# Kernel tuning notes

Hardware: AMD Instinct MI355X
Metric: run time of the kernel (lower is better)

Reference implementation:

```python
import jax, jax.numpy as jnp
import numpy as np

B, R, N, F = 8, 8, 1024, 256


def setup_inputs() -> dict:
    key = jax.random.key(0)
    k1, k2 = jax.random.split(key)
    inputs = jax.random.normal(k1, (B, R, N, F), dtype=jnp.float32)
    Bs = jax.random.normal(k2, (R, F, F), dtype=jnp.float32) * 0.05
    return {"inputs": inputs, "Bs": Bs}


def reference(inputs, Bs):
    # E_r @ B_r : [B,R,N,F] x [R,F,F] -> [B,R,N,F]
    e = jnp.einsum("brnf,rfg->brng", inputs, Bs)
    # (E_r B_r) @ E_r^T : [B,R,N,F] x [B,R,M,F] -> [B,R,N,M]
    scores = jnp.einsum("brng,brmg->brnm", e, inputs)
    return jax.nn.sigmoid(scores)
```

## Files before the change

kernel.cpp:

```cpp
#include <hip/hip_runtime.h>


typedef float   f32x4 __attribute__((ext_vector_type(4)));
typedef _Float16 f16x8 __attribute__((ext_vector_type(8)));

#define WS_E_OFF   0
#define WS_BST_OFF 16777216
#define WS_e_OFF   17301504

__global__ __launch_bounds__(256) void bl_convert(
    const float* __restrict__ E, const float* __restrict__ Bs,
    _Float16* __restrict__ wsE, _Float16* __restrict__ wsBsT) {
  int bid = blockIdx.x, tid = threadIdx.x;
  if (bid < 8192) {
    int cid = (bid << 8) + tid;
    int br  = cid >> 15;
    int rem = cid & 32767;
    int fc  = rem >> 10;
    int n   = rem & 1023;
    const float* src = E + ((size_t)br << 18) + n * 256 + (fc << 3);
    f32x4 v0 = *(const f32x4*)src;
    f32x4 v1 = *(const f32x4*)(src + 4);
    f16x8 h;
    h[0] = (_Float16)v0[0]; h[1] = (_Float16)v0[1];
    h[2] = (_Float16)v0[2]; h[3] = (_Float16)v0[3];
    h[4] = (_Float16)v1[0]; h[5] = (_Float16)v1[1];
    h[6] = (_Float16)v1[2]; h[7] = (_Float16)v1[3];
    *(f16x8*)(wsE + ((size_t)br << 18) + (fc << 13) + (n << 3)) = h;
  } else {
    int cid = ((bid - 8192) << 8) + tid;
    int r   = cid >> 13;
    int rem = cid & 8191;
    int fc  = rem >> 8;
    int g   = rem & 255;
    const float* src = Bs + (r << 16) + (fc << 3) * 256 + g;
    f16x8 h;
#pragma unroll
    for (int j = 0; j < 8; ++j) h[j] = (_Float16)src[j * 256];
    *(f16x8*)(wsBsT + (r << 16) + (fc << 11) + (g << 3)) = h;
  }
}

__global__ __launch_bounds__(256) void bl_gemm1(
    const _Float16* __restrict__ wsE, const _Float16* __restrict__ wsBsT,
    _Float16* __restrict__ wse) {
  __shared__ _Float16 sA[8192];
  __shared__ _Float16 sB[8192];
  int bid = blockIdx.x;
  int br = bid >> 4;
  int t  = bid & 15;
  int n0 = (t >> 1) << 7;
  int g0 = (t & 1) << 7;
  int r  = br & 7;
  int tid  = threadIdx.x;
  int lane = tid & 63, wave = tid >> 6;
  int wm = wave >> 1, wn = wave & 1;
  int quad = lane >> 4, l16 = lane & 15;

  const _Float16* aG = wsE   + ((size_t)br << 18) + (n0 << 3);
  const _Float16* bG = wsBsT + (r << 16) + (g0 << 3);

  f32x4 acc[4][4] = {};

  for (int kk = 0; kk < 4; ++kk) {
    __syncthreads();
#pragma unroll
    for (int i = 0; i < 4; ++i) {
      int c = (i << 8) + tid;
      int kcl = c >> 7, nl = c & 127;
      *(f16x8*)&sA[c << 3] = *(const f16x8*)(aG + (((kk << 3) + kcl) << 13) + (nl << 3));
    }
#pragma unroll
    for (int i = 0; i < 4; ++i) {
      int c = (i << 8) + tid;
      int kcl = c >> 7, gl = c & 127;
      *(f16x8*)&sB[c << 3] = *(const f16x8*)(bG + (((kk << 3) + kcl) << 11) + (gl << 3));
    }
    __syncthreads();
#pragma unroll
    for (int ks = 0; ks < 2; ++ks) {
      int kc = (ks << 2) + quad;
      f16x8 af[4], bf[4];
#pragma unroll
      for (int rt = 0; rt < 4; ++rt)
        af[rt] = *(const f16x8*)&sA[((kc << 7) + (wm << 6) + (rt << 4) + l16) << 3];
#pragma unroll
      for (int ct = 0; ct < 4; ++ct)
        bf[ct] = *(const f16x8*)&sB[((kc << 7) + (wn << 6) + (ct << 4) + l16) << 3];
#pragma unroll
      for (int rt = 0; rt < 4; ++rt)
#pragma unroll
        for (int ct = 0; ct < 4; ++ct)
          acc[rt][ct] = __builtin_amdgcn_mfma_f32_16x16x32_f16(af[rt], bf[ct], acc[rt][ct], 0, 0, 0);
    }
  }
  _Float16* eB = wse + ((size_t)br << 18);
#pragma unroll
  for (int rt = 0; rt < 4; ++rt) {
#pragma unroll
    for (int ct = 0; ct < 4; ++ct) {
      int g  = g0 + (wn << 6) + (ct << 4) + l16;
      int gc = g >> 3, gj = g & 7;
#pragma unroll
      for (int i = 0; i < 4; ++i) {
        int n = n0 + (wm << 6) + (rt << 4) + (quad << 2) + i;
        eB[(gc << 13) + (n << 3) + gj] = (_Float16)acc[rt][ct][i];
      }
    }
  }
}

__global__ __launch_bounds__(256) void bl_gemm2(
    const _Float16* __restrict__ wse, const _Float16* __restrict__ wsE,
    float* __restrict__ out) {
  __shared__ _Float16 sA[8192];
  __shared__ _Float16 sB[8192];
  int bid = blockIdx.x;
  int br = bid >> 6;
  int t  = bid & 63;
  int n0 = (t >> 3) << 7;
  int m0 = (t & 7) << 7;
  int tid  = threadIdx.x;
  int lane = tid & 63, wave = tid >> 6;
  int wm = wave >> 1, wn = wave & 1;
  int quad = lane >> 4, l16 = lane & 15;

  const _Float16* aG = wse + ((size_t)br << 18) + (n0 << 3);
  const _Float16* bG = wsE + ((size_t)br << 18) + (m0 << 3);

  f32x4 acc[4][4] = {};

  for (int kk = 0; kk < 4; ++kk) {
    __syncthreads();
#pragma unroll
    for (int i = 0; i < 4; ++i) {
      int c = (i << 8) + tid;
      int kcl = c >> 7, nl = c & 127;
      *(f16x8*)&sA[c << 3] = *(const f16x8*)(aG + (((kk << 3) + kcl) << 13) + (nl << 3));
    }
#pragma unroll
    for (int i = 0; i < 4; ++i) {
      int c = (i << 8) + tid;
      int kcl = c >> 7, ml = c & 127;
      *(f16x8*)&sB[c << 3] = *(const f16x8*)(bG + (((kk << 3) + kcl) << 13) + (ml << 3));
    }
    __syncthreads();
#pragma unroll
    for (int ks = 0; ks < 2; ++ks) {
      int kc = (ks << 2) + quad;
      f16x8 af[4], bf[4];
#pragma unroll
      for (int rt = 0; rt < 4; ++rt)
        af[rt] = *(const f16x8*)&sA[((kc << 7) + (wm << 6) + (rt << 4) + l16) << 3];
#pragma unroll
      for (int ct = 0; ct < 4; ++ct)
        bf[ct] = *(const f16x8*)&sB[((kc << 7) + (wn << 6) + (ct << 4) + l16) << 3];
#pragma unroll
      for (int rt = 0; rt < 4; ++rt)
#pragma unroll
        for (int ct = 0; ct < 4; ++ct)
          acc[rt][ct] = __builtin_amdgcn_mfma_f32_16x16x32_f16(af[rt], bf[ct], acc[rt][ct], 0, 0, 0);
    }
  }
  float* oB = out + ((size_t)br << 20);
#pragma unroll
  for (int rt = 0; rt < 4; ++rt) {
#pragma unroll
    for (int ct = 0; ct < 4; ++ct) {
      int m = m0 + (wn << 6) + (ct << 4) + l16;
#pragma unroll
      for (int i = 0; i < 4; ++i) {
        int n = n0 + (wm << 6) + (rt << 4) + (quad << 2) + i;
        float x = acc[rt][ct][i];
        float s = __builtin_amdgcn_rcpf(1.0f + __expf(-x));
        oB[((size_t)n << 10) + m] = s;
      }
    }
  }
}

extern "C" void kernel_launch(void* const* d_in, const int* in_sizes, int n_in,
                              void* d_out, int out_size, void* d_ws, size_t ws_size,
                              hipStream_t stream) {
  const float* E  = (const float*)d_in[0];
  const float* Bs = (const float*)d_in[1];
  _Float16* wsE   = (_Float16*)d_ws + WS_E_OFF;
  _Float16* wsBsT = (_Float16*)d_ws + WS_BST_OFF;
  _Float16* wse   = (_Float16*)d_ws + WS_e_OFF;
  float* out = (float*)d_out;

  bl_convert<<<8448, 256, 0, stream>>>(E, Bs, wsE, wsBsT);
  bl_gemm1<<<1024, 256, 0, stream>>>(wsE, wsBsT, wse);
  bl_gemm2<<<4096, 256, 0, stream>>>(wse, wsE, out);
}
```

Measured before the change: 388.8 us.

## Swap MFMA operands for vectorized epilogue stores, prefetch tiles, remap block order

```diff
diff --git a/kernel.cpp b/kernel.cpp
--- a/kernel.cpp
+++ b/kernel.cpp
@@ -1,8 +1,9 @@
 #include <hip/hip_runtime.h>
 
 
-typedef float   f32x4 __attribute__((ext_vector_type(4)));
+typedef float    f32x4 __attribute__((ext_vector_type(4)));
 typedef _Float16 f16x8 __attribute__((ext_vector_type(8)));
+typedef _Float16 f16x4 __attribute__((ext_vector_type(4)));
 
 #define WS_E_OFF   0
 #define WS_BST_OFF 16777216
@@ -46,7 +47,8 @@
     _Float16* __restrict__ wse) {
   __shared__ _Float16 sA[8192];
   __shared__ _Float16 sB[8192];
-  int bid = blockIdx.x;
+  int b0  = blockIdx.x;
+  int bid = ((b0 & 7) << 7) + (b0 >> 3);
   int br = bid >> 4;
   int t  = bid & 15;
   int n0 = (t >> 1) << 7;
@@ -63,18 +65,25 @@
   f32x4 acc[4][4] = {};
 
   for (int kk = 0; kk < 4; ++kk) {
-    __syncthreads();
+    f16x8 va[4], vb[4];
 #pragma unroll
     for (int i = 0; i < 4; ++i) {
       int c = (i << 8) + tid;
       int kcl = c >> 7, nl = c & 127;
-      *(f16x8*)&sA[c << 3] = *(const f16x8*)(aG + (((kk << 3) + kcl) << 13) + (nl << 3));
+      va[i] = *(const f16x8*)(aG + (((kk << 3) + kcl) << 13) + (nl << 3));
     }
 #pragma unroll
     for (int i = 0; i < 4; ++i) {
       int c = (i << 8) + tid;
       int kcl = c >> 7, gl = c & 127;
-      *(f16x8*)&sB[c << 3] = *(const f16x8*)(bG + (((kk << 3) + kcl) << 11) + (gl << 3));
+      vb[i] = *(const f16x8*)(bG + (((kk << 3) + kcl) << 11) + (gl << 3));
+    }
+    __syncthreads();
+#pragma unroll
+    for (int i = 0; i < 4; ++i) {
+      int c = (i << 8) + tid;
+      *(f16x8*)&sA[c << 3] = va[i];
+      *(f16x8*)&sB[c << 3] = vb[i];
     }
     __syncthreads();
 #pragma unroll
@@ -91,21 +100,21 @@
       for (int rt = 0; rt < 4; ++rt)
 #pragma unroll
         for (int ct = 0; ct < 4; ++ct)
-          acc[rt][ct] = __builtin_amdgcn_mfma_f32_16x16x32_f16(af[rt], bf[ct], acc[rt][ct], 0, 0, 0);
+          acc[rt][ct] = __builtin_amdgcn_mfma_f32_16x16x32_f16(bf[ct], af[rt], acc[rt][ct], 0, 0, 0);
     }
   }
   _Float16* eB = wse + ((size_t)br << 18);
 #pragma unroll
   for (int rt = 0; rt < 4; ++rt) {
+    int n = n0 + (wm << 6) + (rt << 4) + l16;
 #pragma unroll
     for (int ct = 0; ct < 4; ++ct) {
-      int g  = g0 + (wn << 6) + (ct << 4) + l16;
+      int g  = g0 + (wn << 6) + (ct << 4) + (quad << 2);
       int gc = g >> 3, gj = g & 7;
-#pragma unroll
-      for (int i = 0; i < 4; ++i) {
-        int n = n0 + (wm << 6) + (rt << 4) + (quad << 2) + i;
-        eB[(gc << 13) + (n << 3) + gj] = (_Float16)acc[rt][ct][i];
-      }
+      f16x4 h;
+#pragma unroll
+      for (int i = 0; i < 4; ++i) h[i] = (_Float16)acc[rt][ct][i];
+      *(f16x4*)(eB + (gc << 13) + (n << 3) + gj) = h;
     }
   }
 }
@@ -115,7 +124,8 @@
     float* __restrict__ out) {
   __shared__ _Float16 sA[8192];
   __shared__ _Float16 sB[8192];
-  int bid = blockIdx.x;
+  int b0  = blockIdx.x;
+  int bid = ((b0 & 7) << 9) + (b0 >> 3);
   int br = bid >> 6;
   int t  = bid & 63;
   int n0 = (t >> 3) << 7;
@@ -131,18 +141,25 @@
   f32x4 acc[4][4] = {};
 
   for (int kk = 0; kk < 4; ++kk) {
-    __syncthreads();
+    f16x8 va[4], vb[4];
 #pragma unroll
     for (int i = 0; i < 4; ++i) {
       int c = (i << 8) + tid;
       int kcl = c >> 7, nl = c & 127;
-      *(f16x8*)&sA[c << 3] = *(const f16x8*)(aG + (((kk << 3) + kcl) << 13) + (nl << 3));
+      va[i] = *(const f16x8*)(aG + (((kk << 3) + kcl) << 13) + (nl << 3));
     }
 #pragma unroll
     for (int i = 0; i < 4; ++i) {
       int c = (i << 8) + tid;
       int kcl = c >> 7, ml = c & 127;
-      *(f16x8*)&sB[c << 3] = *(const f16x8*)(bG + (((kk << 3) + kcl) << 13) + (ml << 3));
+      vb[i] = *(const f16x8*)(bG + (((kk << 3) + kcl) << 13) + (ml << 3));
+    }
+    __syncthreads();
+#pragma unroll
+    for (int i = 0; i < 4; ++i) {
+      int c = (i << 8) + tid;
+      *(f16x8*)&sA[c << 3] = va[i];
+      *(f16x8*)&sB[c << 3] = vb[i];
     }
     __syncthreads();
 #pragma unroll
@@ -159,22 +176,23 @@
       for (int rt = 0; rt < 4; ++rt)
 #pragma unroll
         for (int ct = 0; ct < 4; ++ct)
-          acc[rt][ct] = __builtin_amdgcn_mfma_f32_16x16x32_f16(af[rt], bf[ct], acc[rt][ct], 0, 0, 0);
+          acc[rt][ct] = __builtin_amdgcn_mfma_f32_16x16x32_f16(bf[ct], af[rt], acc[rt][ct], 0, 0, 0);
     }
   }
   float* oB = out + ((size_t)br << 20);
 #pragma unroll
   for (int rt = 0; rt < 4; ++rt) {
+    int n = n0 + (wm << 6) + (rt << 4) + l16;
 #pragma unroll
     for (int ct = 0; ct < 4; ++ct) {
-      int m = m0 + (wn << 6) + (ct << 4) + l16;
+      int m = m0 + (wn << 6) + (ct << 4) + (quad << 2);
+      f32x4 v;
 #pragma unroll
       for (int i = 0; i < 4; ++i) {
-        int n = n0 + (wm << 6) + (rt << 4) + (quad << 2) + i;
         float x = acc[rt][ct][i];
-        float s = __builtin_amdgcn_rcpf(1.0f + __expf(-x));
-        oB[((size_t)n << 10) + m] = s;
+        v[i] = __builtin_amdgcn_rcpf(1.0f + __expf(-x));
       }
+      *(f32x4*)(oB + ((size_t)n << 10) + m) = v;
     }
   }
 }
```

Measured after the change: 366.2 us. 5.8% less time.
